# Kernel optimization log

Measured on AMD Instinct MI355X. Metric: run time of the kernel, lower is better.

Reference implementation:

```python
import jax, jax.numpy as jnp
import numpy as np


def setup_inputs() -> dict:
    key = jax.random.key(0)
    ks = jax.random.split(key, 13)
    B, T, F, H = 512, 128, 256, 128
    X = jax.random.normal(ks[0], (B, T, F), jnp.float32)
    miss = jax.random.uniform(ks[1], (B, T, F)) < 0.3
    X = jnp.where(miss, -1.0, X)  # -1 marks missing values (GRU-D convention)
    X_last = jax.random.normal(ks[2], (B, T, F), jnp.float32)

    def u(k, shape, fan):
        s = 1.0 / np.sqrt(fan)
        return jax.random.uniform(k, shape, jnp.float32, -s, s)

    return {
        'X': X, 'X_last': X_last,
        'W_x': u(ks[3], (F, F), F), 'b_x': u(ks[4], (F,), F),
        'W_h': u(ks[5], (H, F), F), 'b_h': u(ks[6], (H,), F),
        'W_ih': u(ks[7], (4 * H, F), H), 'b_ih': u(ks[8], (4 * H,), H),
        'W_hh': u(ks[9], (4 * H, H), H), 'b_hh': u(ks[10], (4 * H,), H),
        'W_attn': u(ks[11], (1, 2 * H + 2 * T), 2 * H + 2 * T),
        'b_attn': u(ks[12], (1,), 2 * H + 2 * T),
    }


def reference(X, X_last, W_x, b_x, W_h, b_h, W_ih, b_ih, W_hh, b_hh, W_attn, b_attn):
    B, T, F = X.shape
    H = W_h.shape[0]

    mask = (X != -1.0).astype(X.dtype)           # [B,T,F] 1=observed
    X0 = jnp.where(mask > 0, X, 0.0)             # X with -1 -> 0 (in-place mutation in torch)

    # deltaX recurrence: d[0]=0; d[t] = 1 if observed at t-1 else d[t-1]+1
    def dstep(d, m_prev):
        d = jnp.where(m_prev > 0, jnp.ones_like(d), d + 1.0)
        return d, d
    m_xs = jnp.transpose(mask[:, :-1, :], (1, 0, 2))            # [T-1,B,F]
    _, d_rest = jax.lax.scan(dstep, jnp.zeros((B, F), X.dtype), m_xs)
    deltaX = jnp.concatenate([jnp.zeros((1, B, F), X.dtype), d_rest], 0)
    deltaX = jnp.transpose(deltaX, (1, 0, 2))                   # [B,T,F]

    # per-feature empirical mean over observed steps
    count = mask.sum(1)
    X_mean = jnp.where(count > 0, X0.sum(1) / jnp.maximum(count, 1.0), 0.0)  # [B,F]

    # decays: FilterLinear with identity filter -> diagonal weight only
    w_x_diag = jnp.diagonal(W_x)
    dx = jnp.exp(-jax.nn.relu(deltaX * w_x_diag + b_x))                       # [B,T,F]
    Dh = jnp.exp(-jax.nn.relu(jnp.einsum('btf,hf->bth', deltaX, W_h) + b_h))  # [B,T,H]

    # GRU-D style imputation (fully vectorized over t)
    X_new = (1.0 - mask) * (dx * X_last + (1.0 - dx) * X_mean[:, None, :]) + mask * X0

    # split attention weights per concat order: [h(H), s(H), X_new(T), mask(T)]
    wa_h = W_attn[0, :H]
    wa_s = W_attn[0, H:2 * H]
    wa_x = W_attn[0, 2 * H:2 * H + T]
    wa_m = W_attn[0, 2 * H + T:]
    # torch fills X_new buffer step-by-step, so at step t entries t'>t are 0:
    # dot over time axis == cumulative sum, precompute once.
    Sx = jnp.cumsum(X_new * wa_x[None, :, None], axis=1)        # [B,T,F]
    c_mask = jnp.einsum('btf,t->bf', mask, wa_m)                # [B,F]

    def step(carry, xs):
        h, c = carry                       # [B,H], [B,H]
        Dh_t, Sx_t, X0_t = xs
        h = Dh_t * h                       # hidden-state decay
        score = (h @ wa_h + c @ wa_s + b_attn[0])[:, None] + Sx_t + c_mask  # [B,F]
        alpha = jax.nn.softmax(score, axis=1)
        x_t = alpha * X0_t                 # attention-weighted input
        gates = x_t @ W_ih.T + b_ih + h @ W_hh.T + b_hh          # [B,4H]
        i, f, g, o = jnp.split(gates, 4, axis=1)
        c = jax.nn.sigmoid(f) * c + jax.nn.sigmoid(i) * jnp.tanh(g)
        h = jax.nn.sigmoid(o) * jnp.tanh(c)
        return (h, c), (x_t, h)

    init = (jnp.zeros((B, H), X.dtype), jnp.zeros((B, H), X.dtype))
    xs = (jnp.transpose(Dh, (1, 0, 2)),
          jnp.transpose(Sx, (1, 0, 2)),
          jnp.transpose(X0, (1, 0, 2)))
    _, (X_tilde, X_enc) = jax.lax.scan(step, init, xs)
    return jnp.transpose(X_tilde, (1, 0, 2)), jnp.transpose(X_enc, (1, 0, 2))
```

## Files before the change

### kernel.cpp

```cpp
#include <hip/hip_runtime.h>
#include <hip/hip_bf16.h>
#include <cmath>

#define BB 512
#define TT 128
#define FF 256
#define HH 128
#define GG 512
#define MM 65536

typedef short bf16x8 __attribute__((ext_vector_type(8)));
typedef float f32x4 __attribute__((ext_vector_type(4)));

__device__ __forceinline__ float sigmf(float x) { return 1.0f / (1.0f + __expf(-x)); }
__device__ __forceinline__ float tanh_fast(float x) {
    return 1.0f - 2.0f / (__expf(2.0f * x) + 1.0f);
}
__device__ __forceinline__ short f2bf(float f) {
    __hip_bfloat16 h = __float2bfloat16(f);
    return *reinterpret_cast<short*>(&h);
}
__device__ __forceinline__ float bf2f(short s) {
    unsigned int u = ((unsigned int)(unsigned short)s) << 16;
    return __uint_as_float(u);
}
__device__ __forceinline__ bf16x8 cvt8(const float* p) {
    bf16x8 r;
#pragma unroll
    for (int i = 0; i < 8; ++i) r[i] = f2bf(p[i]);
    return r;
}

__global__ __launch_bounds__(256) void k1_preprocess(
    const float* __restrict__ X, const float* __restrict__ X_last,
    const float* __restrict__ W_x, const float* __restrict__ b_x,
    const float* __restrict__ W_attn,
    unsigned short* __restrict__ DX, float* __restrict__ SX, float* __restrict__ CM)
{
    const int b = blockIdx.x;
    const int f = threadIdx.x;
    __shared__ float wl[256];
    wl[f] = W_attn[256 + f];
    __syncthreads();

    const float* xb  = X      + (size_t)b * TT * FF + f;
    const float* xlb = X_last + (size_t)b * TT * FF + f;

    unsigned long long mb0 = 0ull, mb1 = 0ull;
    float sum = 0.f, cnt = 0.f, cm = 0.f;
    for (int tb = 0; tb < TT; tb += 16) {
        float xs[16];
#pragma unroll
        for (int i = 0; i < 16; ++i) xs[i] = xb[(tb + i) * FF];
#pragma unroll
        for (int i = 0; i < 16; ++i) {
            int t = tb + i;
            bool m = (xs[i] != -1.0f);
            if (m) {
                sum += xs[i]; cnt += 1.0f;
                if (t < 64) mb0 |= (1ull << t); else mb1 |= (1ull << (t - 64));
            }
            cm += (m ? 1.0f : 0.0f) * wl[128 + t];
        }
    }
    const float mean = (cnt > 0.f) ? (sum / cnt) : 0.f;
    CM[(size_t)b * FF + f] = cm;

    const float wxd = W_x[(size_t)f * FF + f];
    const float bx  = b_x[f];
    unsigned short* dxb = DX + (size_t)b * TT * FF + f;
    float* sxb = SX + (size_t)b * TT * FF + f;

    float d = 0.f, s = 0.f;
    bool mprev = false;
    for (int tb = 0; tb < TT; tb += 8) {
        float xv[8], xlv[8];
#pragma unroll
        for (int i = 0; i < 8; ++i) xv[i]  = xb[(tb + i) * FF];
#pragma unroll
        for (int i = 0; i < 8; ++i) xlv[i] = xlb[(tb + i) * FF];
#pragma unroll
        for (int i = 0; i < 8; ++i) {
            int t = tb + i;
            bool m = (t < 64) ? ((mb0 >> t) & 1ull) : ((mb1 >> (t - 64)) & 1ull);
            if (t > 0) d = mprev ? 1.0f : (d + 1.0f);
            mprev = m;
            dxb[t * FF] = (unsigned short)f2bf(d);
            float x0  = m ? xv[i] : 0.f;
            float dxv = __expf(-fmaxf(fmaf(d, wxd, bx), 0.f));
            float xnew = m ? x0 : (dxv * xlv[i] + (1.0f - dxv) * mean);
            s += xnew * wl[t];
            sxb[t * FF] = s;
        }
    }
}

__global__ __launch_bounds__(256) void k2_gemm_dh_mfma(
    const unsigned short* __restrict__ A,
    const float* __restrict__ W,
    const float* __restrict__ bias1,
    float* __restrict__ C)
{
    __shared__ short As[128 * 64];
    __shared__ short Bh[128 * 64];
    __shared__ short Bl[128 * 64];

    const int tid  = threadIdx.x;
    const int lane = tid & 63;
    const int wave = tid >> 6;
    const int wm = wave >> 1, wn = wave & 1;
    const int r0 = blockIdx.x * 128;

    f32x4 acc[4][4] = {};

    for (int kc = 0; kc < 256; kc += 64) {
#pragma unroll
        for (int i = 0; i < 4; ++i) {
            int slot = i * 256 + tid;
            int row = slot >> 3, kg = slot & 7;
            int byte = (row * 128 + kg * 16) ^ ((row & 7) << 4);
            *(bf16x8*)((char*)As + byte) =
                *(const bf16x8*)&A[(size_t)(r0 + row) * 256 + kc + kg * 8];
            float tmp[8];
            *(float4*)&tmp[0] = *(const float4*)&W[(size_t)row * 256 + kc + kg * 8];
            *(float4*)&tmp[4] = *(const float4*)&W[(size_t)row * 256 + kc + kg * 8 + 4];
            bf16x8 hi, lo;
#pragma unroll
            for (int j = 0; j < 8; ++j) {
                hi[j] = f2bf(tmp[j]);
                lo[j] = f2bf(tmp[j] - bf2f(hi[j]));
            }
            *(bf16x8*)((char*)Bh + byte) = hi;
            *(bf16x8*)((char*)Bl + byte) = lo;
        }
        __syncthreads();

#pragma unroll
        for (int ks = 0; ks < 2; ++ks) {
            bf16x8 af[4], bh[4], bl[4];
#pragma unroll
            for (int mf = 0; mf < 4; ++mf) {
                int row = wm * 64 + mf * 16 + (lane & 15);
                int byte = (row * 128 + ks * 64 + (lane >> 4) * 16) ^ ((row & 7) << 4);
                af[mf] = *(const bf16x8*)((const char*)As + byte);
            }
#pragma unroll
            for (int nf = 0; nf < 4; ++nf) {
                int row = wn * 64 + nf * 16 + (lane & 15);
                int byte = (row * 128 + ks * 64 + (lane >> 4) * 16) ^ ((row & 7) << 4);
                bh[nf] = *(const bf16x8*)((const char*)Bh + byte);
                bl[nf] = *(const bf16x8*)((const char*)Bl + byte);
            }
#pragma unroll
            for (int mf = 0; mf < 4; ++mf)
#pragma unroll
                for (int nf = 0; nf < 4; ++nf) {
                    acc[mf][nf] = __builtin_amdgcn_mfma_f32_16x16x32_bf16(
                        af[mf], bh[nf], acc[mf][nf], 0, 0, 0);
                    acc[mf][nf] = __builtin_amdgcn_mfma_f32_16x16x32_bf16(
                        af[mf], bl[nf], acc[mf][nf], 0, 0, 0);
                }
        }
        __syncthreads();
    }

    float b1[4];
#pragma unroll
    for (int nf = 0; nf < 4; ++nf) b1[nf] = bias1[wn * 64 + nf * 16 + (lane & 15)];
#pragma unroll
    for (int mf = 0; mf < 4; ++mf)
#pragma unroll
        for (int nf = 0; nf < 4; ++nf) {
            int col = wn * 64 + nf * 16 + (lane & 15);
#pragma unroll
            for (int reg = 0; reg < 4; ++reg) {
                int row = r0 + wm * 64 + mf * 16 + (lane >> 4) * 4 + reg;
                C[(size_t)row * HH + col] = __expf(-fmaxf(acc[mf][nf][reg] + b1[nf], 0.f));
            }
        }
}

__global__ __launch_bounds__(256) void k3_softmax(
    const float* __restrict__ SX, const float* __restrict__ CM,
    const float* __restrict__ X, float* __restrict__ Xt)
{
    const int tid  = threadIdx.x;
    const int lane = tid & 63;
    const int w    = tid >> 6;
    const int r    = blockIdx.x * 4 + w;
    const int b    = r >> 7;

    const float4 sx = *(const float4*)&SX[(size_t)r * FF + lane * 4];
    const float4 cm = *(const float4*)&CM[(size_t)b * FF + lane * 4];
    float s0 = sx.x + cm.x, s1 = sx.y + cm.y, s2 = sx.z + cm.z, s3 = sx.w + cm.w;

    float mx = fmaxf(fmaxf(s0, s1), fmaxf(s2, s3));
#pragma unroll
    for (int o = 32; o > 0; o >>= 1) mx = fmaxf(mx, __shfl_xor(mx, o));
    float e0 = __expf(s0 - mx), e1 = __expf(s1 - mx);
    float e2 = __expf(s2 - mx), e3 = __expf(s3 - mx);
    float sm = e0 + e1 + e2 + e3;
#pragma unroll
    for (int o = 32; o > 0; o >>= 1) sm += __shfl_xor(sm, o);
    float inv = 1.0f / sm;

    const float4 xv = *(const float4*)&X[(size_t)r * FF + lane * 4];
    float4 o4;
    o4.x = ((xv.x != -1.0f) ? xv.x : 0.f) * e0 * inv;
    o4.y = ((xv.y != -1.0f) ? xv.y : 0.f) * e1 * inv;
    o4.z = ((xv.z != -1.0f) ? xv.z : 0.f) * e2 * inv;
    o4.w = ((xv.w != -1.0f) ? xv.w : 0.f) * e3 * inv;
    *(float4*)&Xt[(size_t)r * FF + lane * 4] = o4;
}

__global__ __launch_bounds__(256) void k4_gemm_bf16(
    const float* __restrict__ A,
    const float* __restrict__ W,
    const float* __restrict__ bias1,
    const float* __restrict__ bias2,
    float* __restrict__ C)
{
    __shared__ short As[128 * 64];
    __shared__ short Bs[128 * 64];

    const int tid  = threadIdx.x;
    const int lane = tid & 63;
    const int wave = tid >> 6;
    const int wm = wave >> 1, wn = wave & 1;
    const int r0 = blockIdx.x * 128;
    const int c0 = blockIdx.y * 128;

    f32x4 acc[4][4] = {};

    for (int kc = 0; kc < 256; kc += 64) {
#pragma unroll
        for (int i = 0; i < 4; ++i) {
            int slot = i * 256 + tid;
            int row = slot >> 3, kg = slot & 7;
            int byte = (row * 128 + kg * 16) ^ ((row & 7) << 4);
            float tmp[8];
            *(float4*)&tmp[0] = *(const float4*)&A[(size_t)(r0 + row) * 256 + kc + kg * 8];
            *(float4*)&tmp[4] = *(const float4*)&A[(size_t)(r0 + row) * 256 + kc + kg * 8 + 4];
            *(bf16x8*)((char*)As + byte) = cvt8(tmp);
            *(float4*)&tmp[0] = *(const float4*)&W[(size_t)(c0 + row) * 256 + kc + kg * 8];
            *(float4*)&tmp[4] = *(const float4*)&W[(size_t)(c0 + row) * 256 + kc + kg * 8 + 4];
            *(bf16x8*)((char*)Bs + byte) = cvt8(tmp);
        }
        __syncthreads();

#pragma unroll
        for (int ks = 0; ks < 2; ++ks) {
            bf16x8 af[4], bw[4];
#pragma unroll
            for (int mf = 0; mf < 4; ++mf) {
                int row = wm * 64 + mf * 16 + (lane & 15);
                int byte = (row * 128 + ks * 64 + (lane >> 4) * 16) ^ ((row & 7) << 4);
                af[mf] = *(const bf16x8*)((const char*)As + byte);
            }
#pragma unroll
            for (int nf = 0; nf < 4; ++nf) {
                int row = wn * 64 + nf * 16 + (lane & 15);
                int byte = (row * 128 + ks * 64 + (lane >> 4) * 16) ^ ((row & 7) << 4);
                bw[nf] = *(const bf16x8*)((const char*)Bs + byte);
            }
#pragma unroll
            for (int mf = 0; mf < 4; ++mf)
#pragma unroll
                for (int nf = 0; nf < 4; ++nf)
                    acc[mf][nf] = __builtin_amdgcn_mfma_f32_16x16x32_bf16(
                        af[mf], bw[nf], acc[mf][nf], 0, 0, 0);
        }
        __syncthreads();
    }

    float bsum[4];
#pragma unroll
    for (int nf = 0; nf < 4; ++nf) {
        int col = c0 + wn * 64 + nf * 16 + (lane & 15);
        bsum[nf] = bias1[col] + bias2[col];
    }
#pragma unroll
    for (int mf = 0; mf < 4; ++mf)
#pragma unroll
        for (int nf = 0; nf < 4; ++nf) {
            int col = c0 + wn * 64 + nf * 16 + (lane & 15);
#pragma unroll
            for (int reg = 0; reg < 4; ++reg) {
                int row = r0 + wm * 64 + mf * 16 + (lane >> 4) * 4 + reg;
                C[(size_t)row * GG + col] = acc[mf][nf][reg] + bsum[nf];
            }
        }
}

__global__ __launch_bounds__(512) void k5_recurrence_mfma(
    const float* __restrict__ Dh, const float* __restrict__ G,
    const float* __restrict__ W_hh, float* __restrict__ Xenc)
{
    __shared__ short hbuf[2][2][2][160];
    const int tid  = threadIdx.x;
    const int lane = tid & 63;
    const int w    = tid >> 6;
    const int b0   = blockIdx.x * 2;
    const int l    = lane & 15;
    const int r    = (lane >> 4) & 1;
    const bool st  = (lane < 32);

    bf16x8 wf[4][4];
#pragma unroll
    for (int q = 0; q < 4; ++q)
#pragma unroll
        for (int ks = 0; ks < 4; ++ks) {
            int gate = q * 128 + w * 16 + l;
            const float* src = &W_hh[(size_t)gate * HH + ks * 32 + (lane >> 4) * 8];
            float tmp[8];
            *(float4*)&tmp[0] = *(const float4*)&src[0];
            *(float4*)&tmp[4] = *(const float4*)&src[4];
            wf[q][ks] = cvt8(tmp);
        }

    for (int i = tid; i < 2 * 2 * 2 * 160; i += 512) ((short*)hbuf)[i] = 0;

    const float* gb = G    + (size_t)(b0 + r) * TT * GG + w * 16 + l;
    const float* db = Dh   + (size_t)(b0 + r) * TT * HH + w * 16 + l;
    float*       xb = Xenc + (size_t)(b0 + r) * TT * HH + w * 16 + l;

    float cst = 0.f;
    float gq0 = gb[0], gq1 = gb[128], gq2 = gb[256], gq3 = gb[384];
    float dnx = db[HH];

    for (int t = 0; t < TT; ++t) {
        __syncthreads();
        const int rb = t & 1;
        f32x4 acc[4] = {};
#pragma unroll
        for (int s = 0; s < 2; ++s)
#pragma unroll
            for (int ks = 0; ks < 4; ++ks) {
                const bf16x8 af =
                    *(const bf16x8*)&hbuf[rb][s][lane & 1][ks * 32 + (lane >> 4) * 8];
#pragma unroll
                for (int q = 0; q < 4; ++q)
                    acc[q] = __builtin_amdgcn_mfma_f32_16x16x32_bf16(af, wf[q][ks], acc[q], 0, 0, 0);
            }

        const int tn  = (t + 1 < TT) ? (t + 1) : (TT - 1);
        const int tn2 = (t + 2 < TT) ? (t + 2) : (TT - 1);
        const float* gp = gb + (size_t)tn * GG;
        float ngq0 = gp[0], ngq1 = gp[128], ngq2 = gp[256], ngq3 = gp[384];
        float ndnx = db[(size_t)tn2 * HH];

        float gi = (r ? acc[0][1] : acc[0][0]) + gq0;
        float gf = (r ? acc[1][1] : acc[1][0]) + gq1;
        float gg = (r ? acc[2][1] : acc[2][0]) + gq2;
        float go = (r ? acc[3][1] : acc[3][0]) + gq3;
        float c = sigmf(gf) * cst + sigmf(gi) * tanh_fast(gg);
        cst = c;
        float h = sigmf(go) * tanh_fast(c);
        float hp = dnx * h;
        short hhi = f2bf(hp);
        short hlo = f2bf(hp - bf2f(hhi));
        if (st) {
            xb[(size_t)t * HH] = h;
            hbuf[rb ^ 1][0][r][w * 16 + l] = hhi;
            hbuf[rb ^ 1][1][r][w * 16 + l] = hlo;
        }
        gq0 = ngq0; gq1 = ngq1; gq2 = ngq2; gq3 = ngq3;
        dnx = ndnx;
    }
}

extern "C" void kernel_launch(void* const* d_in, const int* in_sizes, int n_in,
                              void* d_out, int out_size, void* d_ws, size_t ws_size,
                              hipStream_t stream)
{
    const float* X      = (const float*)d_in[0];
    const float* X_last = (const float*)d_in[1];
    const float* W_x    = (const float*)d_in[2];
    const float* b_x    = (const float*)d_in[3];
    const float* W_h    = (const float*)d_in[4];
    const float* b_h    = (const float*)d_in[5];
    const float* W_ih   = (const float*)d_in[6];
    const float* b_ih   = (const float*)d_in[7];
    const float* W_hh   = (const float*)d_in[8];
    const float* b_hh   = (const float*)d_in[9];
    const float* W_attn = (const float*)d_in[10];

    float* ws = (float*)d_ws;
    unsigned short* DXbf = (unsigned short*)ws;
    float* SX = ws + (size_t)8388608;
    float* Gb = ws;
    float* CM = ws + (size_t)33554432;

    float* Xt   = (float*)d_out;
    float* Xenc = (float*)d_out + (size_t)16777216;
    float* DH   = Xenc;

    k1_preprocess<<<BB, 256, 0, stream>>>(X, X_last, W_x, b_x, W_attn, DXbf, SX, CM);
    k2_gemm_dh_mfma<<<MM / 128, 256, 0, stream>>>(DXbf, W_h, b_h, DH);
    k3_softmax<<<MM / 4, 256, 0, stream>>>(SX, CM, X, Xt);
    k4_gemm_bf16<<<dim3(MM / 128, 4), 256, 0, stream>>>(Xt, W_ih, b_ih, b_hh, Gb);
    k5_recurrence_mfma<<<BB / 2, 512, 0, stream>>>(DH, Gb, W_hh, Xenc);
}
```

Baseline: 472.7 us.

## Double-buffer preprocess loads and unroll recurrence by two with split accumulators

The preprocess kernel now software-pipelines its strided global loads, fetching the next chunk of X and X_last into alternate register buffers while the current chunk is processed. The recurrence kernel is unrolled by two timesteps with compile-time buffer indices. It prefetches gate and decay inputs two steps ahead and replaces __syncthreads with an explicit LDS wait plus s_barrier. The hi and lo MFMA chains now use separate accumulators, which breaks the serial dependency between them at the cost of more registers and an extra add per gate.

```diff
diff --git a/kernel.cpp b/kernel.cpp
--- a/kernel.cpp
+++ b/kernel.cpp
@@ -48,21 +48,34 @@
 
     unsigned long long mb0 = 0ull, mb1 = 0ull;
     float sum = 0.f, cnt = 0.f, cm = 0.f;
-    for (int tb = 0; tb < TT; tb += 16) {
-        float xs[16];
-#pragma unroll
-        for (int i = 0; i < 16; ++i) xs[i] = xb[(tb + i) * FF];
+    float p0[16], p1[16];
+#pragma unroll
+    for (int i = 0; i < 16; ++i) p0[i] = xb[i * FF];
+#define K1P1(ARR, TB)                                                        \
+    {                                                                        \
+        _Pragma("unroll")                                                    \
+        for (int i = 0; i < 16; ++i) {                                       \
+            int t = (TB) + i;                                                \
+            bool m = (ARR[i] != -1.0f);                                      \
+            if (m) {                                                         \
+                sum += ARR[i]; cnt += 1.0f;                                  \
+                if (t < 64) mb0 |= (1ull << t); else mb1 |= (1ull << (t - 64)); \
+            }                                                                \
+            cm += (m ? 1.0f : 0.0f) * wl[128 + t];                           \
+        }                                                                    \
+    }
+    for (int tb = 0; tb < TT; tb += 32) {
+#pragma unroll
+        for (int i = 0; i < 16; ++i) p1[i] = xb[(tb + 16 + i) * FF];
+        K1P1(p0, tb)
 #pragma unroll
         for (int i = 0; i < 16; ++i) {
-            int t = tb + i;
-            bool m = (xs[i] != -1.0f);
-            if (m) {
-                sum += xs[i]; cnt += 1.0f;
-                if (t < 64) mb0 |= (1ull << t); else mb1 |= (1ull << (t - 64));
-            }
-            cm += (m ? 1.0f : 0.0f) * wl[128 + t];
-        }
-    }
+            int tt = tb + 32 + i; tt = (tt < TT) ? tt : (TT - 1);
+            p0[i] = xb[tt * FF];
+        }
+        K1P1(p1, tb + 16)
+    }
+#undef K1P1
     const float mean = (cnt > 0.f) ? (sum / cnt) : 0.f;
     CM[(size_t)b * FF + f] = cm;
 
@@ -73,26 +86,40 @@
 
     float d = 0.f, s = 0.f;
     bool mprev = false;
-    for (int tb = 0; tb < TT; tb += 8) {
-        float xv[8], xlv[8];
-#pragma unroll
-        for (int i = 0; i < 8; ++i) xv[i]  = xb[(tb + i) * FF];
-#pragma unroll
-        for (int i = 0; i < 8; ++i) xlv[i] = xlb[(tb + i) * FF];
+    float xv0[8], xl0[8], xv1[8], xl1[8];
+#pragma unroll
+    for (int i = 0; i < 8; ++i) { xv0[i] = xb[i * FF]; xl0[i] = xlb[i * FF]; }
+#define K1P2(XA, LA, TB)                                                     \
+    {                                                                        \
+        _Pragma("unroll")                                                    \
+        for (int i = 0; i < 8; ++i) {                                        \
+            int t = (TB) + i;                                                \
+            bool m = (t < 64) ? ((mb0 >> t) & 1ull) : ((mb1 >> (t - 64)) & 1ull); \
+            if (t > 0) d = mprev ? 1.0f : (d + 1.0f);                        \
+            mprev = m;                                                       \
+            dxb[t * FF] = (unsigned short)f2bf(d);                           \
+            float x0  = m ? XA[i] : 0.f;                                     \
+            float dxv = __expf(-fmaxf(fmaf(d, wxd, bx), 0.f));               \
+            float xnew = m ? x0 : (dxv * LA[i] + (1.0f - dxv) * mean);       \
+            s += xnew * wl[t];                                               \
+            sxb[t * FF] = s;                                                 \
+        }                                                                    \
+    }
+    for (int tb = 0; tb < TT; tb += 16) {
 #pragma unroll
         for (int i = 0; i < 8; ++i) {
-            int t = tb + i;
-            bool m = (t < 64) ? ((mb0 >> t) & 1ull) : ((mb1 >> (t - 64)) & 1ull);
-            if (t > 0) d = mprev ? 1.0f : (d + 1.0f);
-            mprev = m;
-            dxb[t * FF] = (unsigned short)f2bf(d);
-            float x0  = m ? xv[i] : 0.f;
-            float dxv = __expf(-fmaxf(fmaf(d, wxd, bx), 0.f));
-            float xnew = m ? x0 : (dxv * xlv[i] + (1.0f - dxv) * mean);
-            s += xnew * wl[t];
-            sxb[t * FF] = s;
-        }
-    }
+            int tt = tb + 8 + i;
+            xv1[i] = xb[tt * FF]; xl1[i] = xlb[tt * FF];
+        }
+        K1P2(xv0, xl0, tb)
+#pragma unroll
+        for (int i = 0; i < 8; ++i) {
+            int tt = tb + 16 + i; tt = (tt < TT) ? tt : (TT - 1);
+            xv0[i] = xb[tt * FF]; xl0[i] = xlb[tt * FF];
+        }
+        K1P2(xv1, xl1, tb + 8)
+    }
+#undef K1P2
 }
 
 __global__ __launch_bounds__(256) void k2_gemm_dh_mfma(
@@ -214,10 +241,8 @@
 }
 
 __global__ __launch_bounds__(256) void k4_gemm_bf16(
-    const float* __restrict__ A,
-    const float* __restrict__ W,
-    const float* __restrict__ bias1,
-    const float* __restrict__ bias2,
+    const float* __restrict__ A, const float* __restrict__ W,
+    const float* __restrict__ bias1, const float* __restrict__ bias2,
     float* __restrict__ C)
 {
     __shared__ short As[128 * 64];
@@ -292,6 +317,43 @@
         }
 }
 
+__device__ __forceinline__ void k5_step(
+    int t, int rb, float gq0, float gq1, float gq2, float gq3, float dnx,
+    float& cst, const bf16x8 (&wf)[4][4], short (&hbuf)[2][2][2][160],
+    int lane, int r, int w, int l, bool st, float* __restrict__ xb)
+{
+    asm volatile("s_waitcnt lgkmcnt(0)" ::: "memory");
+    __builtin_amdgcn_s_barrier();
+
+    f32x4 acch[4] = {}, accl[4] = {};
+#pragma unroll
+    for (int ks = 0; ks < 4; ++ks) {
+        const bf16x8 afh = *(const bf16x8*)&hbuf[rb][0][lane & 1][ks * 32 + (lane >> 4) * 8];
+        const bf16x8 afl = *(const bf16x8*)&hbuf[rb][1][lane & 1][ks * 32 + (lane >> 4) * 8];
+#pragma unroll
+        for (int q = 0; q < 4; ++q) {
+            acch[q] = __builtin_amdgcn_mfma_f32_16x16x32_bf16(afh, wf[q][ks], acch[q], 0, 0, 0);
+            accl[q] = __builtin_amdgcn_mfma_f32_16x16x32_bf16(afl, wf[q][ks], accl[q], 0, 0, 0);
+        }
+    }
+
+    float gi = (r ? (acch[0][1] + accl[0][1]) : (acch[0][0] + accl[0][0])) + gq0;
+    float gf = (r ? (acch[1][1] + accl[1][1]) : (acch[1][0] + accl[1][0])) + gq1;
+    float gg = (r ? (acch[2][1] + accl[2][1]) : (acch[2][0] + accl[2][0])) + gq2;
+    float go = (r ? (acch[3][1] + accl[3][1]) : (acch[3][0] + accl[3][0])) + gq3;
+    float c = sigmf(gf) * cst + sigmf(gi) * tanh_fast(gg);
+    cst = c;
+    float h = sigmf(go) * tanh_fast(c);
+    float hp = dnx * h;
+    short hhi = f2bf(hp);
+    short hlo = f2bf(hp - bf2f(hhi));
+    if (st) {
+        xb[(size_t)t * HH] = h;
+        hbuf[rb ^ 1][0][r][w * 16 + l] = hhi;
+        hbuf[rb ^ 1][1][r][w * 16 + l] = hlo;
+    }
+}
+
 __global__ __launch_bounds__(512) void k5_recurrence_mfma(
     const float* __restrict__ Dh, const float* __restrict__ G,
     const float* __restrict__ W_hh, float* __restrict__ Xenc)
@@ -325,47 +387,30 @@
     float*       xb = Xenc + (size_t)(b0 + r) * TT * HH + w * 16 + l;
 
     float cst = 0.f;
-    float gq0 = gb[0], gq1 = gb[128], gq2 = gb[256], gq3 = gb[384];
-    float dnx = db[HH];
-
-    for (int t = 0; t < TT; ++t) {
-        __syncthreads();
-        const int rb = t & 1;
-        f32x4 acc[4] = {};
-#pragma unroll
-        for (int s = 0; s < 2; ++s)
-#pragma unroll
-            for (int ks = 0; ks < 4; ++ks) {
-                const bf16x8 af =
-                    *(const bf16x8*)&hbuf[rb][s][lane & 1][ks * 32 + (lane >> 4) * 8];
-#pragma unroll
-                for (int q = 0; q < 4; ++q)
-                    acc[q] = __builtin_amdgcn_mfma_f32_16x16x32_bf16(af, wf[q][ks], acc[q], 0, 0, 0);
-            }
-
-        const int tn  = (t + 1 < TT) ? (t + 1) : (TT - 1);
-        const int tn2 = (t + 2 < TT) ? (t + 2) : (TT - 1);
-        const float* gp = gb + (size_t)tn * GG;
-        float ngq0 = gp[0], ngq1 = gp[128], ngq2 = gp[256], ngq3 = gp[384];
-        float ndnx = db[(size_t)tn2 * HH];
-
-        float gi = (r ? acc[0][1] : acc[0][0]) + gq0;
-        float gf = (r ? acc[1][1] : acc[1][0]) + gq1;
-        float gg = (r ? acc[2][1] : acc[2][0]) + gq2;
-        float go = (r ? acc[3][1] : acc[3][0]) + gq3;
-        float c = sigmf(gf) * cst + sigmf(gi) * tanh_fast(gg);
-        cst = c;
-        float h = sigmf(go) * tanh_fast(c);
-        float hp = dnx * h;
-        short hhi = f2bf(hp);
-        short hlo = f2bf(hp - bf2f(hhi));
-        if (st) {
-            xb[(size_t)t * HH] = h;
-            hbuf[rb ^ 1][0][r][w * 16 + l] = hhi;
-            hbuf[rb ^ 1][1][r][w * 16 + l] = hlo;
-        }
-        gq0 = ngq0; gq1 = ngq1; gq2 = ngq2; gq3 = ngq3;
-        dnx = ndnx;
+    float gA0 = gb[0], gA1 = gb[128], gA2 = gb[256], gA3 = gb[384];
+    const float* g1p = gb + GG;
+    float gB0 = g1p[0], gB1 = g1p[128], gB2 = g1p[256], gB3 = g1p[384];
+    float dA = db[(size_t)1 * HH];
+    float dB = db[(size_t)2 * HH];
+
+    for (int tp = 0; tp < TT; tp += 2) {
+        const int t2 = (tp + 2 < TT) ? tp + 2 : TT - 1;
+        const int t3 = (tp + 3 < TT) ? tp + 3 : TT - 1;
+        const int d2 = (tp + 3 < TT) ? tp + 3 : TT - 1;
+        const int d3 = (tp + 4 < TT) ? tp + 4 : TT - 1;
+        const float* g2p = gb + (size_t)t2 * GG;
+        const float* g3p = gb + (size_t)t3 * GG;
+        float n20 = g2p[0], n21 = g2p[128], n22 = g2p[256], n23 = g2p[384];
+        float n30 = g3p[0], n31 = g3p[128], n32 = g3p[256], n33 = g3p[384];
+        float nd2 = db[(size_t)d2 * HH];
+        float nd3 = db[(size_t)d3 * HH];
+
+        k5_step(tp,     0, gA0, gA1, gA2, gA3, dA, cst, wf, hbuf, lane, r, w, l, st, xb);
+        k5_step(tp + 1, 1, gB0, gB1, gB2, gB3, dB, cst, wf, hbuf, lane, r, w, l, st, xb);
+
+        gA0 = n20; gA1 = n21; gA2 = n22; gA3 = n23;
+        gB0 = n30; gB1 = n31; gB2 = n32; gB3 = n33;
+        dA = nd2; dB = nd3;
     }
 }
 
```

After: 491.0 us. 3.9% more time.
